# Performance work log

Hardware: AMD Instinct MI355X
Metric: run time of the kernel (lower is better)

Reference implementation:

```python
import jax, jax.numpy as jnp
import numpy as np

EPS = 1e-6

def setup_inputs() -> dict:
    key = jax.random.key(0)
    k1, k2, k3 = jax.random.split(key, 3)
    B, T, D = 64, 2048, 768
    feature = jax.random.normal(k1, (B, T, D), dtype=jnp.float32)
    # base mask logits uniform in [0,1) (all non-negative)
    att_mask = jax.random.uniform(k2, (B, T, 1), dtype=jnp.float32)
    # emulate variable-length utterances: mark a random cutoff frame with a
    # negative logit for most samples (first negative index defines length-1)
    lengths = jax.random.randint(k3, (B,), T // 2, T)  # cutoff positions
    # leave a few samples with no negative entry (full-length path)
    lengths = jnp.where(jnp.arange(B) % 8 == 0, T + 1, lengths)
    t_idx = jnp.arange(T)[None, :]
    neg_marker = (t_idx == (lengths[:, None] - 1)).astype(jnp.float32)
    att_mask = att_mask - 2.0 * neg_marker[:, :, None]
    return {"feature": feature, "att_mask": att_mask}


def reference(feature, att_mask):
    # feature: [B, T, D]; att_mask: [B, T, 1]
    B, T, D = feature.shape
    neg = att_mask[:, :, 0] < 0                      # [B, T]
    has_neg = jnp.any(neg, axis=1)                   # [B]
    first_neg = jnp.argmax(neg, axis=1)              # [B] (0 if none)
    # original: length = first_negative_index + 1, else T
    length = jnp.where(has_neg, first_neg + 1, T)    # [B] int
    valid = (jnp.arange(T)[None, :] < length[:, None]).astype(feature.dtype)  # [B,T]
    inv_len = 1.0 / length.astype(feature.dtype)     # [B]
    # masked mean and mean-of-squares in one pass over feature
    mean_vec = jnp.einsum('btd,bt->bd', feature, valid) * inv_len[:, None]
    meansq = jnp.einsum('btd,bt->bd', feature * feature, valid) * inv_len[:, None]
    var_vec = jnp.sqrt(meansq - mean_vec * mean_vec + EPS)
    return jnp.concatenate([mean_vec, var_vec], axis=-1)  # [B, 2D]
```

## Files before the change

### kernel.cpp

```cpp
#include <hip/hip_runtime.h>
#include <math.h>

#define EPSV 1e-6f

__global__ void len_kernel(const float* __restrict__ mask,
                           int* __restrict__ lens, int T) {
    const int b = blockIdx.x;
    const float* m = mask + (size_t)b * T;
    int local = T;
    if ((T & 3) == 0) {
        const float4* m4 = (const float4*)m;
        const int T4 = T >> 2;
        for (int i = threadIdx.x; i < T4; i += blockDim.x) {
            float4 v = m4[i];
            if (v.x < 0.f) local = min(local, 4 * i);
            if (v.y < 0.f) local = min(local, 4 * i + 1);
            if (v.z < 0.f) local = min(local, 4 * i + 2);
            if (v.w < 0.f) local = min(local, 4 * i + 3);
        }
    } else {
        for (int t = threadIdx.x; t < T; t += blockDim.x)
            if (m[t] < 0.f) local = min(local, t);
    }
    __shared__ int s[256];
    s[threadIdx.x] = local;
    __syncthreads();
    #pragma unroll
    for (int off = 128; off > 0; off >>= 1) {
        if ((int)threadIdx.x < off)
            s[threadIdx.x] = min(s[threadIdx.x], s[threadIdx.x + off]);
        __syncthreads();
    }
    if (threadIdx.x == 0) {
        int first = s[0];
        lens[b] = (first < T) ? (first + 1) : T;
    }
}

__global__ __launch_bounds__(192) void partial_kernel(
        const float* __restrict__ feat,
        const int* __restrict__ lens,
        float4* __restrict__ psum,
        float4* __restrict__ psq,
        int nchunk, int T, int D4) {
    const int c = blockIdx.x;
    const int b = blockIdx.y;
    const int len = lens[b];
    const int t0 = (int)(((long long)c * len) / nchunk);
    const int t1 = (int)(((long long)(c + 1) * len) / nchunk);

    const float4* f = (const float4*)feat + (size_t)b * T * D4;
    const int d4 = threadIdx.x;

    float4 sm = make_float4(0.f, 0.f, 0.f, 0.f);
    float4 sq = make_float4(0.f, 0.f, 0.f, 0.f);

    #pragma unroll 8
    for (int t = t0; t < t1; ++t) {
        float4 v = f[(size_t)t * D4 + d4];
        sm.x += v.x; sm.y += v.y; sm.z += v.z; sm.w += v.w;
        sq.x = fmaf(v.x, v.x, sq.x);
        sq.y = fmaf(v.y, v.y, sq.y);
        sq.z = fmaf(v.z, v.z, sq.z);
        sq.w = fmaf(v.w, v.w, sq.w);
    }

    const size_t slot = ((size_t)b * nchunk + c) * D4 + d4;
    psum[slot] = sm;
    psq[slot]  = sq;
}

__global__ __launch_bounds__(192) void final_kernel(
        const float4* __restrict__ psum,
        const float4* __restrict__ psq,
        const int* __restrict__ lens,
        float* __restrict__ out,
        int nchunk, int D4) {
    const int b  = blockIdx.x;
    const int d4 = threadIdx.x;

    const float4* ps = psum + (size_t)b * nchunk * D4 + d4;
    const float4* pq = psq  + (size_t)b * nchunk * D4 + d4;

    float4 s = make_float4(0.f, 0.f, 0.f, 0.f);
    float4 q = make_float4(0.f, 0.f, 0.f, 0.f);
    #pragma unroll 4
    for (int c = 0; c < nchunk; ++c) {
        float4 v = ps[(size_t)c * D4];
        float4 w = pq[(size_t)c * D4];
        s.x += v.x; s.y += v.y; s.z += v.z; s.w += v.w;
        q.x += w.x; q.y += w.y; q.z += w.z; q.w += w.w;
    }

    const float inv = 1.0f / (float)lens[b];
    float4 mean, var;
    mean.x = s.x * inv; mean.y = s.y * inv; mean.z = s.z * inv; mean.w = s.w * inv;
    var.x = sqrtf(fmaf(-mean.x, mean.x, q.x * inv) + EPSV);
    var.y = sqrtf(fmaf(-mean.y, mean.y, q.y * inv) + EPSV);
    var.z = sqrtf(fmaf(-mean.z, mean.z, q.z * inv) + EPSV);
    var.w = sqrtf(fmaf(-mean.w, mean.w, q.w * inv) + EPSV);

    const int D = D4 * 4;
    float4* orow = (float4*)(out + (size_t)b * 2 * D);
    orow[d4]      = mean;
    orow[D4 + d4] = var;
}

extern "C" void kernel_launch(void* const* d_in, const int* in_sizes, int n_in,
                              void* d_out, int out_size, void* d_ws, size_t ws_size,
                              hipStream_t stream) {
    const float* feature  = (const float*)d_in[0];
    const float* att_mask = (const float*)d_in[1];
    float* out = (float*)d_out;

    const int D  = (int)((long long)in_sizes[0] / in_sizes[1]);
    const int B  = out_size / (2 * D);
    const int T  = in_sizes[1] / B;
    const int D4 = D / 4;

    int nchunk = 64;
    size_t need;
    for (;;) {
        const size_t NS = (size_t)B * nchunk;
        need = 4096 + NS * D4 * sizeof(float4) * 2;
        if (need <= ws_size || nchunk <= 1) break;
        nchunk >>= 1;
    }

    int*    lens = (int*)d_ws;
    float4* psum = (float4*)((char*)d_ws + 4096);
    float4* psq  = psum + (size_t)B * nchunk * D4;

    len_kernel<<<B, 256, 0, stream>>>(att_mask, lens, T);
    dim3 grid(nchunk, B);
    partial_kernel<<<grid, D4, 0, stream>>>(feature, lens, psum, psq,
                                            nchunk, T, D4);
    final_kernel<<<B, D4, 0, stream>>>(psum, psq, lens, out, nchunk, D4);
}
```

Measured before the change: 77.78 us.

## Fuse length scan, partial sums and finalization into one kernel with atomic last-block reduction

```diff
diff --git a/kernel.cpp b/kernel.cpp
--- a/kernel.cpp
+++ b/kernel.cpp
@@ -3,15 +3,26 @@
 
 #define EPSV 1e-6f
 
-__global__ void len_kernel(const float* __restrict__ mask,
-                           int* __restrict__ lens, int T) {
-    const int b = blockIdx.x;
+typedef float f32x4 __attribute__((ext_vector_type(4)));
+
+__global__ __launch_bounds__(192) void fused_kernel(
+        const float* __restrict__ feat,
+        const float* __restrict__ mask,
+        int* __restrict__ ctr,
+        float4* __restrict__ psum,
+        float4* __restrict__ psq,
+        float* __restrict__ out,
+        int nchunk, int T, int D4) {
+    const int c   = blockIdx.x;
+    const int b   = blockIdx.y;
+    const int tid = threadIdx.x;
+
     const float* m = mask + (size_t)b * T;
     int local = T;
     if ((T & 3) == 0) {
         const float4* m4 = (const float4*)m;
         const int T4 = T >> 2;
-        for (int i = threadIdx.x; i < T4; i += blockDim.x) {
+        for (int i = tid; i < T4; i += blockDim.x) {
             float4 v = m4[i];
             if (v.x < 0.f) local = min(local, 4 * i);
             if (v.y < 0.f) local = min(local, 4 * i + 1);
@@ -19,86 +30,71 @@
             if (v.w < 0.f) local = min(local, 4 * i + 3);
         }
     } else {
-        for (int t = threadIdx.x; t < T; t += blockDim.x)
+        for (int t = tid; t < T; t += blockDim.x)
             if (m[t] < 0.f) local = min(local, t);
     }
     __shared__ int s[256];
-    s[threadIdx.x] = local;
+    s[tid] = local;
+    if (tid < 256 - 192) s[192 + tid] = T;
     __syncthreads();
     #pragma unroll
     for (int off = 128; off > 0; off >>= 1) {
-        if ((int)threadIdx.x < off)
-            s[threadIdx.x] = min(s[threadIdx.x], s[threadIdx.x + off]);
+        if (tid < off) s[tid] = min(s[tid], s[tid + off]);
         __syncthreads();
     }
-    if (threadIdx.x == 0) {
-        int first = s[0];
-        lens[b] = (first < T) ? (first + 1) : T;
-    }
-}
+    const int first = s[0];
+    const int len = (first < T) ? (first + 1) : T;
 
-__global__ __launch_bounds__(192) void partial_kernel(
-        const float* __restrict__ feat,
-        const int* __restrict__ lens,
-        float4* __restrict__ psum,
-        float4* __restrict__ psq,
-        int nchunk, int T, int D4) {
-    const int c = blockIdx.x;
-    const int b = blockIdx.y;
-    const int len = lens[b];
     const int t0 = (int)(((long long)c * len) / nchunk);
     const int t1 = (int)(((long long)(c + 1) * len) / nchunk);
 
-    const float4* f = (const float4*)feat + (size_t)b * T * D4;
-    const int d4 = threadIdx.x;
+    const f32x4* f = (const f32x4*)feat + (size_t)b * T * D4;
+    const int d4 = tid;
 
-    float4 sm = make_float4(0.f, 0.f, 0.f, 0.f);
-    float4 sq = make_float4(0.f, 0.f, 0.f, 0.f);
+    f32x4 sm = (f32x4)(0.f);
+    f32x4 sq = (f32x4)(0.f);
 
     #pragma unroll 8
     for (int t = t0; t < t1; ++t) {
-        float4 v = f[(size_t)t * D4 + d4];
-        sm.x += v.x; sm.y += v.y; sm.z += v.z; sm.w += v.w;
-        sq.x = fmaf(v.x, v.x, sq.x);
-        sq.y = fmaf(v.y, v.y, sq.y);
-        sq.z = fmaf(v.z, v.z, sq.z);
-        sq.w = fmaf(v.w, v.w, sq.w);
+        f32x4 v = __builtin_nontemporal_load(f + (size_t)t * D4 + d4);
+        sm += v;
+        sq = v * v + sq;
     }
 
     const size_t slot = ((size_t)b * nchunk + c) * D4 + d4;
-    psum[slot] = sm;
-    psq[slot]  = sq;
-}
+    *(f32x4*)&psum[slot] = sm;
+    *(f32x4*)&psq[slot]  = sq;
 
-__global__ __launch_bounds__(192) void final_kernel(
-        const float4* __restrict__ psum,
-        const float4* __restrict__ psq,
-        const int* __restrict__ lens,
-        float* __restrict__ out,
-        int nchunk, int D4) {
-    const int b  = blockIdx.x;
-    const int d4 = threadIdx.x;
+    __syncthreads();
+    __shared__ int s_last;
+    if (tid == 0) {
+        int prev = __hip_atomic_fetch_add(&ctr[b], 1, __ATOMIC_ACQ_REL,
+                                          __HIP_MEMORY_SCOPE_AGENT);
+        s_last = (prev == nchunk - 1);
+    }
+    __syncthreads();
+    if (!s_last) return;
 
     const float4* ps = psum + (size_t)b * nchunk * D4 + d4;
     const float4* pq = psq  + (size_t)b * nchunk * D4 + d4;
 
-    float4 s = make_float4(0.f, 0.f, 0.f, 0.f);
-    float4 q = make_float4(0.f, 0.f, 0.f, 0.f);
+    float4 S = make_float4(0.f, 0.f, 0.f, 0.f);
+    float4 Q = make_float4(0.f, 0.f, 0.f, 0.f);
     #pragma unroll 4
-    for (int c = 0; c < nchunk; ++c) {
-        float4 v = ps[(size_t)c * D4];
-        float4 w = pq[(size_t)c * D4];
-        s.x += v.x; s.y += v.y; s.z += v.z; s.w += v.w;
-        q.x += w.x; q.y += w.y; q.z += w.z; q.w += w.w;
+    for (int k = 0; k < nchunk; ++k) {
+        float4 v = ps[(size_t)k * D4];
+        float4 w = pq[(size_t)k * D4];
+        S.x += v.x; S.y += v.y; S.z += v.z; S.w += v.w;
+        Q.x += w.x; Q.y += w.y; Q.z += w.z; Q.w += w.w;
     }
 
-    const float inv = 1.0f / (float)lens[b];
+    const float inv = 1.0f / (float)len;
     float4 mean, var;
-    mean.x = s.x * inv; mean.y = s.y * inv; mean.z = s.z * inv; mean.w = s.w * inv;
-    var.x = sqrtf(fmaf(-mean.x, mean.x, q.x * inv) + EPSV);
-    var.y = sqrtf(fmaf(-mean.y, mean.y, q.y * inv) + EPSV);
-    var.z = sqrtf(fmaf(-mean.z, mean.z, q.z * inv) + EPSV);
-    var.w = sqrtf(fmaf(-mean.w, mean.w, q.w * inv) + EPSV);
+    mean.x = S.x * inv; mean.y = S.y * inv; mean.z = S.z * inv; mean.w = S.w * inv;
+    var.x = sqrtf(fmaf(-mean.x, mean.x, Q.x * inv) + EPSV);
+    var.y = sqrtf(fmaf(-mean.y, mean.y, Q.y * inv) + EPSV);
+    var.z = sqrtf(fmaf(-mean.z, mean.z, Q.z * inv) + EPSV);
+    var.w = sqrtf(fmaf(-mean.w, mean.w, Q.w * inv) + EPSV);
 
     const int D = D4 * 4;
     float4* orow = (float4*)(out + (size_t)b * 2 * D);
@@ -118,22 +114,21 @@
     const int T  = in_sizes[1] / B;
     const int D4 = D / 4;
 
-    int nchunk = 64;
+    int nchunk = 16;
     size_t need;
     for (;;) {
-        const size_t NS = (size_t)B * nchunk;
-        need = 4096 + NS * D4 * sizeof(float4) * 2;
+        need = 4096 + (size_t)B * nchunk * D4 * sizeof(float4) * 2;
         if (need <= ws_size || nchunk <= 1) break;
         nchunk >>= 1;
     }
 
-    int*    lens = (int*)d_ws;
+    int*    ctr  = (int*)d_ws;
     float4* psum = (float4*)((char*)d_ws + 4096);
     float4* psq  = psum + (size_t)B * nchunk * D4;
 
-    len_kernel<<<B, 256, 0, stream>>>(att_mask, lens, T);
+    (void)hipMemsetAsync(ctr, 0, 4096, stream);
+
     dim3 grid(nchunk, B);
-    partial_kernel<<<grid, D4, 0, stream>>>(feature, lens, psum, psq,
-                                            nchunk, T, D4);
-    final_kernel<<<B, D4, 0, stream>>>(psum, psq, lens, out, nchunk, D4);
+    fused_kernel<<<grid, D4, 0, stream>>>(feature, att_mask, ctr, psum, psq,
+                                          out, nchunk, T, D4);
 }
```

New measurement: 120.0 us. 1.54x slower.
